# Kernel optimization log

Hardware: AMD Instinct MI355X
Metric: run time of the kernel (lower is better)

The kernel has to match this reference:

```python
import jax, jax.numpy as jnp
import numpy as np

NUM_EXPERTS = 16
HIDDEN = 2048
INTER = 768
TOP_K = 8
TOKENS = 2048
BLOCK = 16  # FP4 quantization block size along the contraction dim

_FP4_LEVELS = jnp.array([0.0, 0.5, 1.0, 1.5, 2.0, 3.0, 4.0, 6.0], dtype=jnp.float32)
_FP4_MIDS = jnp.array([0.25, 0.75, 1.25, 1.75, 2.5, 3.5, 5.0], dtype=jnp.float32)


def fp4_fake_quant(x):
    """Blockwise FP4 (e2m1) quantize-dequantize along the last dim.

    Emulates quantize_to_fp4 + dequant inside fp4_matmul: per-16 block scale
    = amax/6 (6 = max e2m1 magnitude), round-to-nearest on the e2m1 grid.
    """
    shp = x.shape
    xb = x.reshape(shp[:-1] + (shp[-1] // BLOCK, BLOCK))
    amax = jnp.max(jnp.abs(xb), axis=-1, keepdims=True)
    scale = jnp.where(amax > 0, amax / 6.0, 1.0)
    v = xb / scale
    idx = jnp.digitize(jnp.abs(v), _FP4_MIDS)  # 0..7 bucket on e2m1 grid
    q = _FP4_LEVELS[idx] * jnp.sign(v)
    return (q * scale).reshape(shp)


def setup_inputs() -> dict:
    key = jax.random.key(0)
    k1, k2, k3, k4, k5 = jax.random.split(key, 5)
    hidden_states = jax.random.normal(k1, (TOKENS, HIDDEN), dtype=jnp.float32)
    top_k_index = jax.random.randint(k2, (TOKENS, TOP_K), 0, NUM_EXPERTS)
    w = jax.random.uniform(k3, (TOKENS, TOP_K), dtype=jnp.float32) + 1e-3
    top_k_weights = w / jnp.sum(w, axis=-1, keepdims=True)
    gate_up_proj = jax.random.normal(k4, (NUM_EXPERTS, 2 * INTER, HIDDEN), dtype=jnp.float32) * 0.02
    down_proj = jax.random.normal(k5, (NUM_EXPERTS, HIDDEN, INTER), dtype=jnp.float32) * 0.02
    return {
        "hidden_states": hidden_states,
        "top_k_index": top_k_index,
        "top_k_weights": top_k_weights,
        "gate_up_proj": gate_up_proj,
        "down_proj": down_proj,
    }


def reference(hidden_states, top_k_index, top_k_weights, gate_up_proj, down_proj):
    # Combine weight per (token, expert): sums duplicate top-k hits, exactly
    # matching the torch loop's index_add_ over (top_k_pos, token_idx) pairs.
    one_hot = jax.nn.one_hot(top_k_index, NUM_EXPERTS, dtype=hidden_states.dtype)  # [T,k,E]
    w_te = jnp.einsum("tke,tk->te", one_hot, top_k_weights)  # [T,E]

    xq = fp4_fake_quant(hidden_states)                 # activation FP4 (per-row blocks)
    wgu_q = fp4_fake_quant(gate_up_proj)               # [E,2I,H] weight FP4
    wd_q = fp4_fake_quant(down_proj)                   # [E,H,I]

    h = jnp.einsum("th,eoh->eto", xq, wgu_q)           # [E,T,2I]
    gate, up = h[..., :INTER], h[..., INTER:]
    act = jax.nn.silu(gate) * up                       # [E,T,I]
    aq = fp4_fake_quant(act)
    y = jnp.einsum("eti,ehi->eth", aq, wd_q)           # [E,T,H]
    out = jnp.einsum("eth,te->th", y, w_te)            # scatter-combine
    return out
```

## Files before the change

kernel.cpp:

```cpp
#include <hip/hip_runtime.h>
#include <hip/hip_fp16.h>
#include <cstdint>

#define T_TOK 2048
#define H_DIM 2048
#define I_DIM 768
#define N_EXP 16
#define TOPK  8

typedef _Float16 half8  __attribute__((ext_vector_type(8)));
typedef _Float16 half4v __attribute__((ext_vector_type(4)));
typedef float    f32x4  __attribute__((ext_vector_type(4)));

#define GLDS16(g, l)                                                        \
  __builtin_amdgcn_global_load_lds(                                         \
      (const __attribute__((address_space(1))) unsigned int*)(g),           \
      (__attribute__((address_space(3))) unsigned int*)(l), 16, 0, 0)

__device__ __forceinline__ float fp4_q(float x, float scale) {
  float v = x / scale;
  float a = fabsf(v);
  float q;
  if      (a < 0.25f) q = 0.0f;
  else if (a < 0.75f) q = 0.5f;
  else if (a < 1.25f) q = 1.0f;
  else if (a < 1.75f) q = 1.5f;
  else if (a < 2.5f)  q = 2.0f;
  else if (a < 3.5f)  q = 3.0f;
  else if (a < 5.0f)  q = 4.0f;
  else                q = 6.0f;
  return copysignf(q, v) * scale;
}

__device__ __forceinline__ int swz_m(int r) { return (r & 3) ^ ((r >> 2) & 1); }

__global__ void zero_kernel(float* __restrict__ out, int* __restrict__ counts) {
  int gid = blockIdx.x * 256 + threadIdx.x;
  ((f32x4*)out)[gid] = (f32x4){0.f, 0.f, 0.f, 0.f};
  if (gid < N_EXP) counts[gid] = 0;
}

__global__ void router_kernel(const int* __restrict__ idx, const float* __restrict__ wts,
                              float* __restrict__ w_te, int* __restrict__ counts,
                              int* __restrict__ list) {
  int t = blockIdx.x * 256 + threadIdx.x;
  if (t >= T_TOK) return;
  int   id[TOPK];
  float w[TOPK];
#pragma unroll
  for (int k = 0; k < TOPK; ++k) { id[k] = idx[t * TOPK + k]; w[k] = wts[t * TOPK + k]; }
#pragma unroll
  for (int e = 0; e < N_EXP; ++e) {
    float acc = 0.f;
#pragma unroll
    for (int k = 0; k < TOPK; ++k) acc += (id[k] == e) ? w[k] : 0.0f;
    w_te[t * N_EXP + e] = acc;
    if (acc != 0.0f) {
      int pos = atomicAdd(&counts[e], 1);
      list[e * T_TOK + pos] = t;
    }
  }
}

__global__ void quant_kernel(const float* __restrict__ src, _Float16* __restrict__ dh,
                             _Float16* __restrict__ dl, int n4) {
  int gid = blockIdx.x * 256 + threadIdx.x;
  if (gid >= n4) return;
  f32x4 x = ((const f32x4*)src)[gid];
  float am = fmaxf(fmaxf(fabsf(x[0]), fabsf(x[1])), fmaxf(fabsf(x[2]), fabsf(x[3])));
  am = fmaxf(am, __shfl_xor(am, 1, 64));
  am = fmaxf(am, __shfl_xor(am, 2, 64));
  float scale = am > 0.0f ? am / 6.0f : 1.0f;
  half4v hv, lv;
#pragma unroll
  for (int j = 0; j < 4; ++j) {
    float xq = fp4_q(x[j], scale);
    _Float16 h = (_Float16)xq;
    hv[j] = h;
    lv[j] = (_Float16)(xq - (float)h);
  }
  ((half4v*)dh)[gid] = hv;
  if (dl) ((half4v*)dl)[gid] = lv;
}

__launch_bounds__(256, 2)
__global__ void gemm1_kernel(const _Float16* __restrict__ xh, const _Float16* __restrict__ xl,
                             const _Float16* __restrict__ wh, const _Float16* __restrict__ wl,
                             const int* __restrict__ counts, const int* __restrict__ list,
                             _Float16* __restrict__ aq) {
  __shared__ __align__(16) _Float16 smem[2][4][128 * 32];
  __shared__ int s_tok[128];

  const int orig = blockIdx.x;
  const int swz  = (orig & 7) * (3072 / 8) + (orig >> 3);
  const int tile = swz & 15;
  const int n0i  = (swz >> 4) % 12;
  const int e    = swz / 192;

  const int cnt  = counts[e];
  const int row0 = tile * 128;
  if (row0 >= cnt) return;
  const int nvalid = min(128, cnt - row0);
  const int n0  = n0i * 64;
  const int tid = threadIdx.x;
  const int wave = tid >> 6, lane = tid & 63;

  if (tid < 128) {
    int r = (tid < nvalid) ? tid : 0;
    s_tok[tid] = list[e * T_TOK + row0 + r];
  }
  __syncthreads();

  size_t aG[2], bG[2];
  unsigned ldsOff[2];
#pragma unroll
  for (int p = 0; p < 2; ++p) {
    int q = tid + p * 256;
    int r = q >> 2, c = q & 3;
    int sc = c ^ swz_m(r);
    ldsOff[p] = (unsigned)q * 8;
    int tok = s_tok[r];
    aG[p] = ((size_t)tok * H_DIM) * 2 + (size_t)(sc * 16);
    int grow = (r < 64) ? (e * 2 * I_DIM + n0 + r)
                        : (e * 2 * I_DIM + I_DIM + n0 + (r - 64));
    bG[p] = ((size_t)grow * H_DIM) * 2 + (size_t)(sc * 16);
  }

  const int wm = wave >> 1, wn = wave & 1;
  const int kc = lane >> 4;
  unsigned aRd[4], bgRd[2], buRd[2];
#pragma unroll
  for (int fr = 0; fr < 4; ++fr) {
    int R = wm * 64 + fr * 16 + (lane & 15);
    aRd[fr] = (unsigned)(R * 32 + (kc ^ swz_m(R)) * 8);
  }
#pragma unroll
  for (int fn = 0; fn < 2; ++fn) {
    int R = wn * 32 + fn * 16 + (lane & 15);
    bgRd[fn] = (unsigned)(R * 32 + (kc ^ swz_m(R)) * 8);
    int R2 = R + 64;
    buRd[fn] = (unsigned)(R2 * 32 + (kc ^ swz_m(R2)) * 8);
  }

  f32x4 accg[4][2] = {};
  f32x4 accu[4][2] = {};

#define STAGE1(buf, k0)                                                       \
  do {                                                                        \
    size_t kb = (size_t)(k0) * 2;                                             \
    _Pragma("unroll") for (int p = 0; p < 2; ++p) {                           \
      GLDS16((const char*)xh + aG[p] + kb, &smem[buf][0][0] + ldsOff[p]);     \
      GLDS16((const char*)xl + aG[p] + kb, &smem[buf][1][0] + ldsOff[p]);     \
      GLDS16((const char*)wh + bG[p] + kb, &smem[buf][2][0] + ldsOff[p]);     \
      GLDS16((const char*)wl + bG[p] + kb, &smem[buf][3][0] + ldsOff[p]);     \
    }                                                                         \
  } while (0)

  STAGE1(0, 0);
  __syncthreads();
  const int NT = H_DIM / 32;
  for (int t = 0; t < NT; ++t) {
    const int cur = t & 1;
    if (t + 1 < NT) STAGE1(cur ^ 1, (t + 1) * 32);
    const _Float16* sAh = &smem[cur][0][0];
    const _Float16* sAl = &smem[cur][1][0];
    const _Float16* sBh = &smem[cur][2][0];
    const _Float16* sBl = &smem[cur][3][0];
    half8 ah[4], al[4], bgh[2], bgl[2], buh[2], bul[2];
#pragma unroll
    for (int fr = 0; fr < 4; ++fr) {
      ah[fr] = *(const half8*)(sAh + aRd[fr]);
      al[fr] = *(const half8*)(sAl + aRd[fr]);
    }
#pragma unroll
    for (int fn = 0; fn < 2; ++fn) {
      bgh[fn] = *(const half8*)(sBh + bgRd[fn]);
      bgl[fn] = *(const half8*)(sBl + bgRd[fn]);
      buh[fn] = *(const half8*)(sBh + buRd[fn]);
      bul[fn] = *(const half8*)(sBl + buRd[fn]);
    }
#pragma unroll
    for (int fr = 0; fr < 4; ++fr)
#pragma unroll
      for (int fn = 0; fn < 2; ++fn) {
        accg[fr][fn] = __builtin_amdgcn_mfma_f32_16x16x32_f16(ah[fr], bgh[fn], accg[fr][fn], 0, 0, 0);
        accg[fr][fn] = __builtin_amdgcn_mfma_f32_16x16x32_f16(ah[fr], bgl[fn], accg[fr][fn], 0, 0, 0);
        accg[fr][fn] = __builtin_amdgcn_mfma_f32_16x16x32_f16(al[fr], bgh[fn], accg[fr][fn], 0, 0, 0);
        accu[fr][fn] = __builtin_amdgcn_mfma_f32_16x16x32_f16(ah[fr], buh[fn], accu[fr][fn], 0, 0, 0);
        accu[fr][fn] = __builtin_amdgcn_mfma_f32_16x16x32_f16(ah[fr], bul[fn], accu[fr][fn], 0, 0, 0);
        accu[fr][fn] = __builtin_amdgcn_mfma_f32_16x16x32_f16(al[fr], buh[fn], accu[fr][fn], 0, 0, 0);
      }
    __syncthreads();
  }
#undef STAGE1

  _Float16* sStage = &smem[0][0][0];
#pragma unroll
  for (int fr = 0; fr < 4; ++fr)
#pragma unroll
    for (int fn = 0; fn < 2; ++fn) {
      float act[4], am[4];
#pragma unroll
      for (int i = 0; i < 4; ++i) {
        float g = accg[fr][fn][i], u = accu[fr][fn][i];
        float sg = 1.0f / (1.0f + expf(-g));
        act[i] = g * sg * u;
        am[i] = fabsf(act[i]);
      }
#pragma unroll
      for (int m = 1; m < 16; m <<= 1)
#pragma unroll
        for (int i = 0; i < 4; ++i) am[i] = fmaxf(am[i], __shfl_xor(am[i], m, 64));
      int col = wn * 32 + fn * 16 + (lane & 15);
#pragma unroll
      for (int i = 0; i < 4; ++i) {
        float scale = am[i] > 0.0f ? am[i] / 6.0f : 1.0f;
        float qv = fp4_q(act[i], scale);
        int row = wm * 64 + fr * 16 + (lane >> 4) * 4 + i;
        sStage[row * 64 + col] = (_Float16)qv;
      }
    }
  __syncthreads();
#pragma unroll
  for (int s = 0; s < 4; ++s) {
    int idx2 = tid + s * 256;
    int r = idx2 >> 3, c = idx2 & 7;
    if (r < nvalid) {
      *(uint4*)(aq + ((size_t)(e * T_TOK + row0 + r) * I_DIM + n0 + c * 8)) =
          *(const uint4*)(sStage + r * 64 + c * 8);
    }
  }
}

__launch_bounds__(256, 3)
__global__ void gemm2_kernel(const _Float16* __restrict__ aq, const _Float16* __restrict__ wdh,
                             const int* __restrict__ counts, const int* __restrict__ list,
                             const float* __restrict__ w_te, float* __restrict__ out) {
  __shared__ __align__(16) _Float16 smem[2][2][128 * 32];
  __shared__ int   s_trow[128];
  __shared__ float s_wrow[128];

  const int orig = blockIdx.x;
  const int swz  = (orig & 7) * (4096 / 8) + (orig >> 3);
  const int tile = swz & 15;
  const int n1i  = (swz >> 4) & 15;
  const int e    = swz >> 8;

  const int cnt  = counts[e];
  const int row0 = tile * 128;
  if (row0 >= cnt) return;
  const int nvalid = min(128, cnt - row0);
  const int n1  = n1i * 128;
  const int tid = threadIdx.x;
  const int wave = tid >> 6, lane = tid & 63;

  if (tid < 128) {
    int r = (tid < nvalid) ? tid : 0;
    int t = list[e * T_TOK + row0 + r];
    s_trow[tid] = t;
    s_wrow[tid] = w_te[t * N_EXP + e];
  }

  size_t aG[2], bG[2];
  unsigned ldsOff[2];
#pragma unroll
  for (int p = 0; p < 2; ++p) {
    int q = tid + p * 256;
    int r = q >> 2, c = q & 3;
    int sc = c ^ swz_m(r);
    ldsOff[p] = (unsigned)q * 8;
    int ra = (r < nvalid) ? r : 0;
    aG[p] = ((size_t)(e * T_TOK + row0 + ra) * I_DIM) * 2 + (size_t)(sc * 16);
    bG[p] = ((size_t)(e * H_DIM + n1 + r) * I_DIM) * 2 + (size_t)(sc * 16);
  }

  const int wm = wave >> 1, wn = wave & 1;
  const int kc = lane >> 4;
  unsigned aRd[4], bRd[4];
#pragma unroll
  for (int fr = 0; fr < 4; ++fr) {
    int R = wm * 64 + fr * 16 + (lane & 15);
    aRd[fr] = (unsigned)(R * 32 + (kc ^ swz_m(R)) * 8);
  }
#pragma unroll
  for (int fn = 0; fn < 4; ++fn) {
    int R = wn * 64 + fn * 16 + (lane & 15);
    bRd[fn] = (unsigned)(R * 32 + (kc ^ swz_m(R)) * 8);
  }

  f32x4 acc[4][4] = {};

#define STAGE2(buf, k0)                                                       \
  do {                                                                        \
    size_t kb = (size_t)(k0) * 2;                                             \
    _Pragma("unroll") for (int p = 0; p < 2; ++p) {                           \
      GLDS16((const char*)aq  + aG[p] + kb, &smem[buf][0][0] + ldsOff[p]);    \
      GLDS16((const char*)wdh + bG[p] + kb, &smem[buf][1][0] + ldsOff[p]);    \
    }                                                                         \
  } while (0)

  STAGE2(0, 0);
  __syncthreads();
  const int NT = I_DIM / 32;
  for (int t = 0; t < NT; ++t) {
    const int cur = t & 1;
    if (t + 1 < NT) STAGE2(cur ^ 1, (t + 1) * 32);
    const _Float16* sA = &smem[cur][0][0];
    const _Float16* sB = &smem[cur][1][0];
    half8 a[4], b[4];
#pragma unroll
    for (int fr = 0; fr < 4; ++fr) a[fr] = *(const half8*)(sA + aRd[fr]);
#pragma unroll
    for (int fn = 0; fn < 4; ++fn) b[fn] = *(const half8*)(sB + bRd[fn]);
#pragma unroll
    for (int fr = 0; fr < 4; ++fr)
#pragma unroll
      for (int fn = 0; fn < 4; ++fn)
        acc[fr][fn] = __builtin_amdgcn_mfma_f32_16x16x32_f16(a[fr], b[fn], acc[fr][fn], 0, 0, 0);
    __syncthreads();
  }
#undef STAGE2

#pragma unroll
  for (int fr = 0; fr < 4; ++fr) {
    int rb = wm * 64 + fr * 16 + (lane >> 4) * 4;
#pragma unroll
    for (int i = 0; i < 4; ++i) {
      int row = rb + i;
      if (row < nvalid) {
        int t = s_trow[row];
        float w = s_wrow[row];
#pragma unroll
        for (int fn = 0; fn < 4; ++fn) {
          int col = n1 + wn * 64 + fn * 16 + (lane & 15);
          unsafeAtomicAdd(&out[(size_t)t * H_DIM + col], w * acc[fr][fn][i]);
        }
      }
    }
  }
}

extern "C" void kernel_launch(void* const* d_in, const int* in_sizes, int n_in,
                              void* d_out, int out_size, void* d_ws, size_t ws_size,
                              hipStream_t stream) {
  const float* hs  = (const float*)d_in[0];
  const int*   tki = (const int*)d_in[1];
  const float* tkw = (const float*)d_in[2];
  const float* wgu = (const float*)d_in[3];
  const float* wd  = (const float*)d_in[4];
  float* out = (float*)d_out;

  char* ws = (char*)d_ws;
  size_t off = 0;
  auto alloc = [&](size_t bytes) -> void* {
    void* p = ws + off;
    off += bytes;
    off = (off + 255) & ~(size_t)255;
    return p;
  };
  int*      counts = (int*)alloc(N_EXP * 4);
  float*    w_te   = (float*)alloc((size_t)T_TOK * N_EXP * 4);
  int*      list   = (int*)alloc((size_t)N_EXP * T_TOK * 4);
  _Float16* xh     = (_Float16*)alloc((size_t)T_TOK * H_DIM * 2);
  _Float16* xl     = (_Float16*)alloc((size_t)T_TOK * H_DIM * 2);
  _Float16* wguh   = (_Float16*)alloc((size_t)N_EXP * 2 * I_DIM * H_DIM * 2);
  _Float16* wgul   = (_Float16*)alloc((size_t)N_EXP * 2 * I_DIM * H_DIM * 2);
  _Float16* wdh    = (_Float16*)alloc((size_t)N_EXP * H_DIM * I_DIM * 2);
  _Float16* aqb    = (_Float16*)alloc((size_t)N_EXP * T_TOK * I_DIM * 2);
  if (off > ws_size) return;

  zero_kernel<<<dim3(4096), dim3(256), 0, stream>>>(out, counts);
  router_kernel<<<dim3(8), dim3(256), 0, stream>>>(tki, tkw, w_te, counts, list);
  quant_kernel<<<dim3(4096), dim3(256), 0, stream>>>(hs, xh, xl, T_TOK * H_DIM / 4);
  quant_kernel<<<dim3(49152), dim3(256), 0, stream>>>(wgu, wguh, wgul, N_EXP * 2 * I_DIM * H_DIM / 4);
  quant_kernel<<<dim3(24576), dim3(256), 0, stream>>>(wd, wdh, (_Float16*)nullptr, N_EXP * H_DIM * I_DIM / 4);
  gemm1_kernel<<<dim3(3072), dim3(256), 0, stream>>>(xh, xl, wguh, wgul, counts, list, aqb);
  gemm2_kernel<<<dim3(4096), dim3(256), 0, stream>>>(aqb, wdh, counts, list, w_te, out);
}
```

Measured before the change: 822.9 us.

## Switch gemm1 to single-buffered 64-wide K tiles with 8-way XOR swizzle

The gate/up GEMM loses its double-buffered 32-wide K pipeline and instead loads 64-wide K tiles into a single LDS buffer, with a barrier before and after each load. The XOR swizzle widens to 8 chunks per row to suit the new 128-byte row stride. This halves the number of loop iterations and barriers per tile while keeping the same total LDS footprint, but global loads no longer overlap with MFMA compute inside a block. It therefore depends on the two resident blocks per CU to hide load latency.

```diff
diff --git a/kernel.cpp b/kernel.cpp
--- a/kernel.cpp
+++ b/kernel.cpp
@@ -32,8 +32,6 @@
   return copysignf(q, v) * scale;
 }
 
-__device__ __forceinline__ int swz_m(int r) { return (r & 3) ^ ((r >> 2) & 1); }
-
 __global__ void zero_kernel(float* __restrict__ out, int* __restrict__ counts) {
   int gid = blockIdx.x * 256 + threadIdx.x;
   ((f32x4*)out)[gid] = (f32x4){0.f, 0.f, 0.f, 0.f};
@@ -88,7 +86,10 @@
                              const _Float16* __restrict__ wh, const _Float16* __restrict__ wl,
                              const int* __restrict__ counts, const int* __restrict__ list,
                              _Float16* __restrict__ aq) {
-  __shared__ __align__(16) _Float16 smem[2][4][128 * 32];
+  __shared__ __align__(16) _Float16 sAh[128 * 64];
+  __shared__ __align__(16) _Float16 sAl[128 * 64];
+  __shared__ __align__(16) _Float16 sBh[128 * 64];
+  __shared__ __align__(16) _Float16 sBl[128 * 64];
   __shared__ int s_tok[128];
 
   const int orig = blockIdx.x;
@@ -111,16 +112,15 @@
   }
   __syncthreads();
 
-  size_t aG[2], bG[2];
-  unsigned ldsOff[2];
-#pragma unroll
-  for (int p = 0; p < 2; ++p) {
+  size_t aG[4], bG[4];
+  unsigned ldsOff[4];
+#pragma unroll
+  for (int p = 0; p < 4; ++p) {
     int q = tid + p * 256;
-    int r = q >> 2, c = q & 3;
-    int sc = c ^ swz_m(r);
+    int r = q >> 3, c = q & 7;
+    int sc = c ^ (r & 7);
     ldsOff[p] = (unsigned)q * 8;
-    int tok = s_tok[r];
-    aG[p] = ((size_t)tok * H_DIM) * 2 + (size_t)(sc * 16);
+    aG[p] = ((size_t)s_tok[r] * H_DIM) * 2 + (size_t)(sc * 16);
     int grow = (r < 64) ? (e * 2 * I_DIM + n0 + r)
                         : (e * 2 * I_DIM + I_DIM + n0 + (r - 64));
     bG[p] = ((size_t)grow * H_DIM) * 2 + (size_t)(sc * 16);
@@ -128,73 +128,73 @@
 
   const int wm = wave >> 1, wn = wave & 1;
   const int kc = lane >> 4;
-  unsigned aRd[4], bgRd[2], buRd[2];
+  unsigned aRd[4][2], bgRd[2][2], buRd[2][2];
 #pragma unroll
   for (int fr = 0; fr < 4; ++fr) {
     int R = wm * 64 + fr * 16 + (lane & 15);
-    aRd[fr] = (unsigned)(R * 32 + (kc ^ swz_m(R)) * 8);
+#pragma unroll
+    for (int ks = 0; ks < 2; ++ks)
+      aRd[fr][ks] = (unsigned)(R * 64 + (((ks * 4 + kc) ^ (R & 7)) * 8));
   }
 #pragma unroll
   for (int fn = 0; fn < 2; ++fn) {
-    int R = wn * 32 + fn * 16 + (lane & 15);
-    bgRd[fn] = (unsigned)(R * 32 + (kc ^ swz_m(R)) * 8);
-    int R2 = R + 64;
-    buRd[fn] = (unsigned)(R2 * 32 + (kc ^ swz_m(R2)) * 8);
+    int Rg = wn * 32 + fn * 16 + (lane & 15);
+    int Ru = Rg + 64;
+#pragma unroll
+    for (int ks = 0; ks < 2; ++ks) {
+      bgRd[fn][ks] = (unsigned)(Rg * 64 + (((ks * 4 + kc) ^ (Rg & 7)) * 8));
+      buRd[fn][ks] = (unsigned)(Ru * 64 + (((ks * 4 + kc) ^ (Ru & 7)) * 8));
+    }
   }
 
   f32x4 accg[4][2] = {};
   f32x4 accu[4][2] = {};
 
-#define STAGE1(buf, k0)                                                       \
-  do {                                                                        \
-    size_t kb = (size_t)(k0) * 2;                                             \
-    _Pragma("unroll") for (int p = 0; p < 2; ++p) {                           \
-      GLDS16((const char*)xh + aG[p] + kb, &smem[buf][0][0] + ldsOff[p]);     \
-      GLDS16((const char*)xl + aG[p] + kb, &smem[buf][1][0] + ldsOff[p]);     \
-      GLDS16((const char*)wh + bG[p] + kb, &smem[buf][2][0] + ldsOff[p]);     \
-      GLDS16((const char*)wl + bG[p] + kb, &smem[buf][3][0] + ldsOff[p]);     \
-    }                                                                         \
-  } while (0)
-
-  STAGE1(0, 0);
+  const int NT = H_DIM / 64;
+  for (int t = 0; t < NT; ++t) {
+    __syncthreads();
+    {
+      size_t kb = (size_t)t * 128;
+#pragma unroll
+      for (int p = 0; p < 4; ++p) {
+        GLDS16((const char*)xh + aG[p] + kb, sAh + ldsOff[p]);
+        GLDS16((const char*)xl + aG[p] + kb, sAl + ldsOff[p]);
+        GLDS16((const char*)wh + bG[p] + kb, sBh + ldsOff[p]);
+        GLDS16((const char*)wl + bG[p] + kb, sBl + ldsOff[p]);
+      }
+    }
+    __syncthreads();
+#pragma unroll
+    for (int ks = 0; ks < 2; ++ks) {
+      half8 ah[4], al[4], bgh[2], bgl[2], buh[2], bul[2];
+#pragma unroll
+      for (int fr = 0; fr < 4; ++fr) {
+        ah[fr] = *(const half8*)(sAh + aRd[fr][ks]);
+        al[fr] = *(const half8*)(sAl + aRd[fr][ks]);
+      }
+#pragma unroll
+      for (int fn = 0; fn < 2; ++fn) {
+        bgh[fn] = *(const half8*)(sBh + bgRd[fn][ks]);
+        bgl[fn] = *(const half8*)(sBl + bgRd[fn][ks]);
+        buh[fn] = *(const half8*)(sBh + buRd[fn][ks]);
+        bul[fn] = *(const half8*)(sBl + buRd[fn][ks]);
+      }
+#pragma unroll
+      for (int fr = 0; fr < 4; ++fr)
+#pragma unroll
+        for (int fn = 0; fn < 2; ++fn) {
+          accg[fr][fn] = __builtin_amdgcn_mfma_f32_16x16x32_f16(ah[fr], bgh[fn], accg[fr][fn], 0, 0, 0);
+          accg[fr][fn] = __builtin_amdgcn_mfma_f32_16x16x32_f16(ah[fr], bgl[fn], accg[fr][fn], 0, 0, 0);
+          accg[fr][fn] = __builtin_amdgcn_mfma_f32_16x16x32_f16(al[fr], bgh[fn], accg[fr][fn], 0, 0, 0);
+          accu[fr][fn] = __builtin_amdgcn_mfma_f32_16x16x32_f16(ah[fr], buh[fn], accu[fr][fn], 0, 0, 0);
+          accu[fr][fn] = __builtin_amdgcn_mfma_f32_16x16x32_f16(ah[fr], bul[fn], accu[fr][fn], 0, 0, 0);
+          accu[fr][fn] = __builtin_amdgcn_mfma_f32_16x16x32_f16(al[fr], buh[fn], accu[fr][fn], 0, 0, 0);
+        }
+    }
+  }
+
   __syncthreads();
-  const int NT = H_DIM / 32;
-  for (int t = 0; t < NT; ++t) {
-    const int cur = t & 1;
-    if (t + 1 < NT) STAGE1(cur ^ 1, (t + 1) * 32);
-    const _Float16* sAh = &smem[cur][0][0];
-    const _Float16* sAl = &smem[cur][1][0];
-    const _Float16* sBh = &smem[cur][2][0];
-    const _Float16* sBl = &smem[cur][3][0];
-    half8 ah[4], al[4], bgh[2], bgl[2], buh[2], bul[2];
-#pragma unroll
-    for (int fr = 0; fr < 4; ++fr) {
-      ah[fr] = *(const half8*)(sAh + aRd[fr]);
-      al[fr] = *(const half8*)(sAl + aRd[fr]);
-    }
-#pragma unroll
-    for (int fn = 0; fn < 2; ++fn) {
-      bgh[fn] = *(const half8*)(sBh + bgRd[fn]);
-      bgl[fn] = *(const half8*)(sBl + bgRd[fn]);
-      buh[fn] = *(const half8*)(sBh + buRd[fn]);
-      bul[fn] = *(const half8*)(sBl + buRd[fn]);
-    }
-#pragma unroll
-    for (int fr = 0; fr < 4; ++fr)
-#pragma unroll
-      for (int fn = 0; fn < 2; ++fn) {
-        accg[fr][fn] = __builtin_amdgcn_mfma_f32_16x16x32_f16(ah[fr], bgh[fn], accg[fr][fn], 0, 0, 0);
-        accg[fr][fn] = __builtin_amdgcn_mfma_f32_16x16x32_f16(ah[fr], bgl[fn], accg[fr][fn], 0, 0, 0);
-        accg[fr][fn] = __builtin_amdgcn_mfma_f32_16x16x32_f16(al[fr], bgh[fn], accg[fr][fn], 0, 0, 0);
-        accu[fr][fn] = __builtin_amdgcn_mfma_f32_16x16x32_f16(ah[fr], buh[fn], accu[fr][fn], 0, 0, 0);
-        accu[fr][fn] = __builtin_amdgcn_mfma_f32_16x16x32_f16(ah[fr], bul[fn], accu[fr][fn], 0, 0, 0);
-        accu[fr][fn] = __builtin_amdgcn_mfma_f32_16x16x32_f16(al[fr], buh[fn], accu[fr][fn], 0, 0, 0);
-      }
-    __syncthreads();
-  }
-#undef STAGE1
-
-  _Float16* sStage = &smem[0][0][0];
+  _Float16* sStage = sAh;
 #pragma unroll
   for (int fr = 0; fr < 4; ++fr)
 #pragma unroll
@@ -231,6 +231,8 @@
     }
   }
 }
+
+__device__ __forceinline__ int swz_m(int r) { return (r & 3) ^ ((r >> 2) & 1); }
 
 __launch_bounds__(256, 3)
 __global__ void gemm2_kernel(const _Float16* __restrict__ aq, const _Float16* __restrict__ wdh,
```

New measurement: 777.2 us. 1.06x faster.
